# Kernel tuning notes

Hardware: AMD Instinct MI355X
Metric: run time of the kernel (lower is better)

## Reference

```python
import jax, jax.numpy as jnp
import numpy as np

B, S, H, NH = 2, 2048, 1024, 16
DH = H // NH  # 64

def setup_inputs() -> dict:
    key = jax.random.key(0)
    ks = jax.random.split(key, 6)
    return {
        "hidden_states": jax.random.normal(ks[0], (B, S, H), jnp.float32),
        "attention_mask": jnp.zeros((B, 1, 1, S), jnp.float32),  # additive mask (0 = attend)
        "local_attention_mask": jax.random.randint(ks[1], (B, 1, S, S), 0, 2).astype(jnp.int32),
        "gate_outputs": jax.random.uniform(ks[2], (B, NH, S, 1), jnp.float32),
        "Wq": jax.random.normal(ks[3], (H, H), jnp.float32) * 0.02,
        "bq": jnp.zeros((H,), jnp.float32),
        "Wk": jax.random.normal(ks[4], (H, H), jnp.float32) * 0.02,
        "bk": jnp.zeros((H,), jnp.float32),
        "Wv": jax.random.normal(ks[5], (H, H), jnp.float32) * 0.02,
        "bv": jnp.zeros((H,), jnp.float32),
    }

def _heads(x):
    # [B,S,H] -> [B,NH,S,DH]
    return x.reshape(B, S, NH, DH).transpose(0, 2, 1, 3)

def reference(hidden_states, attention_mask, local_attention_mask, gate_outputs, Wq, bq, Wk, bk, Wv, bv):
    q = _heads(hidden_states @ Wq.T + bq)
    k = _heads(hidden_states @ Wk.T + bk)
    v = _heads(hidden_states @ Wv.T + bv)
    scores = jnp.einsum("bhqd,bhkd->bhqk", q, k) / jnp.sqrt(jnp.float32(DH))
    # global branch (additive mask)
    probs_g = jax.nn.softmax(scores + attention_mask, axis=-1)
    ctx_g = jnp.einsum("bhqk,bhkd->bhqd", probs_g, v)
    # local branch: 0/1 mask -> additive -inf mask
    lmask = (1.0 - local_attention_mask.astype(jnp.float32)) * jnp.finfo(jnp.float32).min
    probs_l = jax.nn.softmax(scores + lmask, axis=-1)
    ctx_l = jnp.einsum("bhqk,bhkd->bhqd", probs_l, v)
    ctx = gate_outputs * ctx_l + (1.0 - gate_outputs) * ctx_g  # [B,NH,S,DH]
    return ctx.transpose(0, 2, 1, 3).reshape(B, S, H)
```

## Files before the change

### kernel.cpp

```cpp
#include <hip/hip_runtime.h>
#include <cstdint>
#include <cstddef>

typedef short short8 __attribute__((ext_vector_type(8)));
typedef float floatx4 __attribute__((ext_vector_type(4)));
typedef unsigned short ushort4v __attribute__((ext_vector_type(4)));
typedef unsigned int uintx4 __attribute__((ext_vector_type(4)));

constexpr int B_ = 2, S_ = 2048, H_ = 1024, NH_ = 16, DH_ = 64;
constexpr int K_ = H_;

__device__ __forceinline__ unsigned short f2bf(float f) {
  unsigned u = __float_as_uint(f);
  u += 0x7fffu + ((u >> 16) & 1u);
  return (unsigned short)(u >> 16);
}

__device__ __forceinline__ unsigned cvtpk(float a, float b) {
  unsigned r;
  asm("v_cvt_pk_bf16_f32 %0, %1, %2" : "=v"(r) : "v"(a), "v"(b));
  return r;
}

__global__ __launch_bounds__(256) void prep_kernel(
    const float* __restrict__ hs, unsigned short* __restrict__ hbf,
    const float* __restrict__ Wq, const float* __restrict__ Wk, const float* __restrict__ Wv,
    unsigned short* __restrict__ wqb, unsigned short* __restrict__ wkb,
    unsigned short* __restrict__ wvb,
    const int* __restrict__ lm, unsigned long long* __restrict__ bm,
    const float* __restrict__ am, float* __restrict__ ea) {
  const int bid = blockIdx.x, tid = threadIdx.x;
  if (bid < 1792) {
    const float* in;
    unsigned short* out;
    int off;
    if (bid < 1024) { in = hs; out = hbf; off = bid; }
    else {
      int wsel = (bid - 1024) >> 8;
      in = (wsel == 0) ? Wq : (wsel == 1) ? Wk : Wv;
      out = (wsel == 0) ? wqb : (wsel == 1) ? wkb : wvb;
      off = (bid - 1024) & 255;
    }
    const int base = off * 4096;
#pragma unroll
    for (int j = 0; j < 4; j++) {
      int i = base + j * 1024 + tid * 4;
      float4 v = *reinterpret_cast<const float4*>(in + i);
      ushort4v o;
      o.x = f2bf(v.x); o.y = f2bf(v.y); o.z = f2bf(v.z); o.w = f2bf(v.w);
      *reinterpret_cast<ushort4v*>(out + i) = o;
    }
  } else if (bid < 9984) {
    const int wbase = (bid - 1792) * 16 + (tid >> 6) * 4;
    const int lane = tid & 63;
#pragma unroll
    for (int j = 0; j < 4; j++) {
      unsigned long long bits = __ballot(lm[(size_t)(wbase + j) * 64 + lane] != 0);
      if (lane == 0) bm[wbase + j] = bits;
    }
  } else {
#pragma unroll
    for (int j = 0; j < 4; j++) {
      int i = j * 1024 + tid * 4;
      float4 v = *reinterpret_cast<const float4*>(am + i);
      float4 o;
      o.x = __expf(v.x); o.y = __expf(v.y); o.z = __expf(v.z); o.w = __expf(v.w);
      *reinterpret_cast<float4*>(ea + i) = o;
    }
  }
}

typedef __attribute__((address_space(1))) const void gvoid;
typedef __attribute__((address_space(3))) void lvoid;
__device__ __forceinline__ void async16(const unsigned short* gp, unsigned short* lp) {
  __builtin_amdgcn_global_load_lds((gvoid*)gp, (lvoid*)lp, 16, 0, 0);
}

__global__ __launch_bounds__(256) void gemm_qkv(
    const unsigned short* __restrict__ A,
    const unsigned short* __restrict__ Wq, const unsigned short* __restrict__ Wk,
    const unsigned short* __restrict__ Wv,
    const float* __restrict__ bq, const float* __restrict__ bk, const float* __restrict__ bv,
    unsigned short* __restrict__ qo, unsigned short* __restrict__ ko,
    unsigned short* __restrict__ vo) {
  __shared__ alignas(16) unsigned short As[128 * 32];
  __shared__ alignas(16) unsigned short Bs[128 * 32];
  const int z = blockIdx.z;
  const unsigned short* W = (z == 0) ? Wq : (z == 1) ? Wk : Wv;
  const float* bias = (z == 0) ? bq : (z == 1) ? bk : bv;

  const int m0 = blockIdx.x * 128, n0 = blockIdx.y * 128;
  const int tid = threadIdx.x, lane = tid & 63, wvi = tid >> 6;
  const int wr = wvi >> 1, wc = wvi & 1, quad = lane >> 4, l16 = lane & 15;

  floatx4 zf = {0.f, 0.f, 0.f, 0.f};
  floatx4 acc[4][4];
  for (int i = 0; i < 4; i++)
    for (int j = 0; j < 4; j++) acc[i][j] = zf;

  for (int kk = 0; kk < K_; kk += 32) {
#pragma unroll
    for (int i = 0; i < 2; i++) {
      int cb = wvi * 128 + i * 64;
      int c = cb + lane;
      int row = c >> 2, kc = c & 3;
      async16(A + (size_t)(m0 + row) * K_ + kk + kc * 8, As + cb * 8);
      async16(W + (size_t)(n0 + row) * K_ + kk + kc * 8, Bs + cb * 8);
    }
    __syncthreads();
    short8 af[4], bfr[4];
#pragma unroll
    for (int mf = 0; mf < 4; mf++)
      af[mf] = *reinterpret_cast<const short8*>(&As[(wr * 64 + mf * 16 + l16) * 32 + quad * 8]);
#pragma unroll
    for (int nf = 0; nf < 4; nf++)
      bfr[nf] = *reinterpret_cast<const short8*>(&Bs[(wc * 64 + nf * 16 + l16) * 32 + quad * 8]);
    if (z == 2) {
#pragma unroll
      for (int mf = 0; mf < 4; mf++)
#pragma unroll
        for (int nf = 0; nf < 4; nf++)
          acc[mf][nf] = __builtin_amdgcn_mfma_f32_16x16x32_bf16(af[mf], bfr[nf], acc[mf][nf], 0, 0, 0);
    } else {
#pragma unroll
      for (int mf = 0; mf < 4; mf++)
#pragma unroll
        for (int nf = 0; nf < 4; nf++)
          acc[mf][nf] = __builtin_amdgcn_mfma_f32_16x16x32_bf16(bfr[nf], af[mf], acc[mf][nf], 0, 0, 0);
    }
    __syncthreads();
  }

  if (z == 2) {
#pragma unroll
    for (int mf = 0; mf < 4; mf++) {
      int mbase = m0 + wr * 64 + mf * 16 + quad * 4;
      int b = mbase >> 11, s0 = mbase & 2047;
      int kl = s0 & 63;
#pragma unroll
      for (int nf = 0; nf < 4; nf++) {
        int n = n0 + wc * 64 + nf * 16 + l16;
        int h = n >> 6, d = n & 63;
        int bh = b * NH_ + h;
        float bvv = bias[n];
        floatx4 c = acc[mf][nf];
        size_t base = (size_t)bh * 131072 + (s0 >> 6) * 4096 + (d >> 4) * 1024 +
                      (kl >> 5) * 512 + ((kl >> 3) & 3) * 128 + (d & 15) * 8 + (kl & 7);
        ushort4v p;
        p.x = f2bf(c[0] + bvv); p.y = f2bf(c[1] + bvv);
        p.z = f2bf(c[2] + bvv); p.w = f2bf(c[3] + bvv);
        *reinterpret_cast<ushort4v*>(&vo[base]) = p;
      }
    }
  } else {
#pragma unroll
    for (int mf = 0; mf < 4; mf++) {
      int s = m0 + wr * 64 + mf * 16 + l16;
      int b = s >> 11;
      int sq = s & 2047;
#pragma unroll
      for (int nf = 0; nf < 4; nf++) {
        int nn = n0 + wc * 64 + nf * 16 + quad * 4;
        int h = nn >> 6, dh = nn & 63;
        int bh = b * NH_ + h;
        float4 b4 = *reinterpret_cast<const float4*>(bias + nn);
        floatx4 c = acc[mf][nf];
        if (z == 0) {
          ushort4v p;
          p.x = f2bf((c[0] + b4.x) * 0.18033688011112042f);
          p.y = f2bf((c[1] + b4.y) * 0.18033688011112042f);
          p.z = f2bf((c[2] + b4.z) * 0.18033688011112042f);
          p.w = f2bf((c[3] + b4.w) * 0.18033688011112042f);
          *reinterpret_cast<ushort4v*>(&qo[((size_t)bh * S_ + sq) * DH_ + dh]) = p;
        } else {
          int kl = sq & 63;
          int t = ((kl >> 4) & 2) | ((kl >> 2) & 1);
          int rr = ((kl >> 1) & 12) | (kl & 3);
          size_t base = (size_t)bh * 131072 + (sq >> 6) * 4096 + t * 1024 +
                        (dh >> 5) * 512 + ((dh >> 3) & 3) * 128 + rr * 8 + (dh & 7);
          ushort4v p;
          p.x = f2bf(c[0] + b4.x); p.y = f2bf(c[1] + b4.y);
          p.z = f2bf(c[2] + b4.z); p.w = f2bf(c[3] + b4.w);
          *reinterpret_cast<ushort4v*>(&ko[base]) = p;
        }
      }
    }
  }
}

__global__ __launch_bounds__(256, 4) void attn_kernel(
    const unsigned short* __restrict__ q,
    const unsigned short* __restrict__ kperm,
    const unsigned short* __restrict__ vperm,
    const float* __restrict__ eam,
    const unsigned long long* __restrict__ bm,
    const float* __restrict__ gate,
    float* __restrict__ out) {
  __shared__ alignas(16) unsigned short Ks[2][4096];
  __shared__ alignas(16) unsigned short Vs[2][4096];

  const int flat = blockIdx.x;
  const int h = (flat & 7) + 8 * ((flat >> 3) & 1);
  const int b = (flat >> 4) & 1;
  const int qt = flat >> 5;
  const int tid = threadIdx.x, lane = tid & 63, wvi = tid >> 6;
  const int quad = lane >> 4, l16 = lane & 15;
  const int bh = b * NH_ + h;
  const int q0 = qt * 64 + wvi * 16;
  const int quad8 = quad * 8;

  const unsigned short* qrow = q + ((size_t)bh * S_ + q0 + l16) * DH_;
  short8 qf0 = *reinterpret_cast<const short8*>(qrow + quad * 8);
  short8 qf1 = *reinterpret_cast<const short8*>(qrow + 32 + quad * 8);

  floatx4 zf = {0.f, 0.f, 0.f, 0.f};
  float psg = 0.f, psl = 0.f;
  floatx4 accg[4], accl[4];
#pragma unroll
  for (int i = 0; i < 4; i++) { accg[i] = zf; accl[i] = zf; }

  const unsigned short* kp = kperm + (size_t)bh * 131072;
  const unsigned short* vp = vperm + (size_t)bh * 131072;
  const float* eamb = eam + (size_t)b * S_;
  const unsigned long long* bmq = bm + ((size_t)b * S_ + q0 + l16) * (S_ / 64);

  const int soA = tid * 8, soB = 2048 + tid * 8;
  const unsigned short* kgA = kp + soA;
  const unsigned short* kgB = kp + soB;
  const unsigned short* vgA = vp + soA;
  const unsigned short* vgB = vp + soB;

  uint4 pk0 = *reinterpret_cast<const uint4*>(kgA);
  uint4 pk1 = *reinterpret_cast<const uint4*>(kgB);
  uint4 pv0 = *reinterpret_cast<const uint4*>(vgA);
  uint4 pv1 = *reinterpret_cast<const uint4*>(vgB);
  *reinterpret_cast<uint4*>(&Ks[0][soA]) = pk0;
  *reinterpret_cast<uint4*>(&Ks[0][soB]) = pk1;
  *reinterpret_cast<uint4*>(&Vs[0][soA]) = pv0;
  *reinterpret_cast<uint4*>(&Vs[0][soB]) = pv1;
  pk0 = *reinterpret_cast<const uint4*>(kgA + 4096);
  pk1 = *reinterpret_cast<const uint4*>(kgB + 4096);
  pv0 = *reinterpret_cast<const uint4*>(vgA + 4096);
  pv1 = *reinterpret_cast<const uint4*>(vgB + 4096);

  for (int kt = 0; kt < S_ / 64; kt++) {
    __syncthreads();
    {
      const int bn = (kt + 1) & 1;
      *reinterpret_cast<uint4*>(&Ks[bn][soA]) = pk0;
      *reinterpret_cast<uint4*>(&Ks[bn][soB]) = pk1;
      *reinterpret_cast<uint4*>(&Vs[bn][soA]) = pv0;
      *reinterpret_cast<uint4*>(&Vs[bn][soB]) = pv1;
    }
    {
      const int tb = ((kt + 2) & 31) * 4096;
      pk0 = *reinterpret_cast<const uint4*>(kgA + tb);
      pk1 = *reinterpret_cast<const uint4*>(kgB + tb);
      pv0 = *reinterpret_cast<const uint4*>(vgA + tb);
      pv1 = *reinterpret_cast<const uint4*>(vgB + tb);
    }
    const int k0 = kt * 64;
    uint2 wv = *reinterpret_cast<const uint2*>(&bmq[kt]);
    unsigned wq0 = wv.x >> quad8;
    unsigned wq1 = wv.y >> quad8;
    float4 ea0 = *reinterpret_cast<const float4*>(eamb + k0 + quad8);
    float4 ea1 = *reinterpret_cast<const float4*>(eamb + k0 + 4 + quad8);
    float4 ea2 = *reinterpret_cast<const float4*>(eamb + k0 + 32 + quad8);
    float4 ea3 = *reinterpret_cast<const float4*>(eamb + k0 + 36 + quad8);

    const unsigned short* Kc = Ks[kt & 1];
    const unsigned short* Vc = Vs[kt & 1];
    floatx4 scT[4];
#pragma unroll
    for (int t = 0; t < 4; t++) {
      const unsigned short* kr = Kc + t * 1024 + lane * 8;
      short8 kf0 = *reinterpret_cast<const short8*>(kr);
      short8 kf1 = *reinterpret_cast<const short8*>(kr + 512);
      scT[t] = __builtin_amdgcn_mfma_f32_16x16x32_bf16(kf0, qf0, zf, 0, 0, 0);
      scT[t] = __builtin_amdgcn_mfma_f32_16x16x32_bf16(kf1, qf1, scT[t], 0, 0, 0);
    }
    uintx4 fgv[2], flv[2];
#pragma unroll
    for (int t = 0; t < 4; t++) {
      const int T = t >> 1, tau = t & 1;
      floatx4 sc = scT[t];
      unsigned wq = T ? wq1 : wq0;
      float4 ea = (t == 0) ? ea0 : (t == 1) ? ea1 : (t == 2) ? ea2 : ea3;
      unsigned m4 = (wq >> (tau * 4)) & 0xFu;
      float e0 = __builtin_amdgcn_exp2f(sc[0]);
      float e1 = __builtin_amdgcn_exp2f(sc[1]);
      float e2 = __builtin_amdgcn_exp2f(sc[2]);
      float e3 = __builtin_amdgcn_exp2f(sc[3]);
      float g0 = e0 * ea.x, g1 = e1 * ea.y, g2 = e2 * ea.z, g3 = e3 * ea.w;
      psg += (g0 + g1) + (g2 + g3);
      float l0 = (m4 & 1u) ? e0 : 0.f;
      float l1 = (m4 & 2u) ? e1 : 0.f;
      float l2 = (m4 & 4u) ? e2 : 0.f;
      float l3 = (m4 & 8u) ? e3 : 0.f;
      psl += (l0 + l1) + (l2 + l3);
      fgv[T][tau * 2]     = cvtpk(g0, g1);
      fgv[T][tau * 2 + 1] = cvtpk(g2, g3);
      flv[T][tau * 2]     = cvtpk(l0, l1);
      flv[T][tau * 2 + 1] = cvtpk(l2, l3);
    }
    short8 FG0 = __builtin_bit_cast(short8, fgv[0]);
    short8 FG1 = __builtin_bit_cast(short8, fgv[1]);
    short8 FL0 = __builtin_bit_cast(short8, flv[0]);
    short8 FL1 = __builtin_bit_cast(short8, flv[1]);
#pragma unroll
    for (int d = 0; d < 4; d++) {
      const unsigned short* vb = Vc + d * 1024 + lane * 8;
      short8 v0 = *reinterpret_cast<const short8*>(vb);
      short8 v1 = *reinterpret_cast<const short8*>(vb + 512);
      accg[d] = __builtin_amdgcn_mfma_f32_16x16x32_bf16(v0, FG0, accg[d], 0, 0, 0);
      accl[d] = __builtin_amdgcn_mfma_f32_16x16x32_bf16(v0, FL0, accl[d], 0, 0, 0);
      accg[d] = __builtin_amdgcn_mfma_f32_16x16x32_bf16(v1, FG1, accg[d], 0, 0, 0);
      accl[d] = __builtin_amdgcn_mfma_f32_16x16x32_bf16(v1, FL1, accl[d], 0, 0, 0);
    }
  }

  float lgf = psg;
  lgf += __shfl_xor(lgf, 16, 64);
  lgf += __shfl_xor(lgf, 32, 64);
  float llf = psl;
  llf += __shfl_xor(llf, 16, 64);
  llf += __shfl_xor(llf, 32, 64);
  const int s = q0 + l16;
  const float g = gate[(size_t)bh * S_ + s];
  const float cg = (1.f - g) / lgf, cl = g / llf;
  float* orow = out + ((size_t)b * S_ + s) * H_ + h * DH_ + quad * 4;
#pragma unroll
  for (int d = 0; d < 4; d++) {
    float4 o;
    o.x = cl * accl[d][0] + cg * accg[d][0];
    o.y = cl * accl[d][1] + cg * accg[d][1];
    o.z = cl * accl[d][2] + cg * accg[d][2];
    o.w = cl * accl[d][3] + cg * accg[d][3];
    *reinterpret_cast<float4*>(orow + d * 16) = o;
  }
}

extern "C" void kernel_launch(void* const* d_in, const int* in_sizes, int n_in,
                              void* d_out, int out_size, void* d_ws, size_t ws_size,
                              hipStream_t stream) {
  (void)in_sizes; (void)n_in; (void)out_size; (void)ws_size;
  const float* hs = (const float*)d_in[0];
  const float* am = (const float*)d_in[1];
  const int* lm = (const int*)d_in[2];
  const float* gate = (const float*)d_in[3];
  const float* Wq = (const float*)d_in[4];
  const float* bq = (const float*)d_in[5];
  const float* Wk = (const float*)d_in[6];
  const float* bk = (const float*)d_in[7];
  const float* Wv = (const float*)d_in[8];
  const float* bv = (const float*)d_in[9];
  float* out = (float*)d_out;

  unsigned short* ws = (unsigned short*)d_ws;
  unsigned short* hbf = ws;
  unsigned short* wqb = hbf + 4194304;
  unsigned short* wkb = wqb + 1048576;
  unsigned short* wvb = wkb + 1048576;
  unsigned short* qb = wvb + 1048576;
  unsigned short* kb = qb + 4194304;
  unsigned short* vtb = kb + 4194304;
  unsigned long long* bmp = (unsigned long long*)(vtb + 4194304);
  float* eamp = (float*)(bmp + 131072);

  prep_kernel<<<9985, 256, 0, stream>>>(hs, hbf, Wq, Wk, Wv, wqb, wkb, wvb, lm, bmp, am, eamp);
  gemm_qkv<<<dim3(32, 8, 3), 256, 0, stream>>>(hbf, wqb, wkb, wvb, bq, bk, bv, qb, kb, vtb);
  attn_kernel<<<dim3(1024), 256, 0, stream>>>(qb, kb, vtb, eamp, bmp, gate, out);
}
```

Before: 229.5 us.

## Move mask preprocessing into GEMM launch and double K-step per sync

The local-mask bit-packing and attention-mask exponentiation blocks move out of the prep kernel and are appended as extra blocks of the QKV GEMM launch, so that memory-bound work can overlap with the GEMM tiles. The GEMM now loads 64 K-elements per iteration into two LDS halves, halving the number of barriers per tile. This doubles LDS use per block, which may lower occupancy. The 1D grid also reorders the GEMM tiles and puts the mask blocks after them, which could delay the GEMM's tail.

```diff
diff --git a/kernel.cpp b/kernel.cpp
--- a/kernel.cpp
+++ b/kernel.cpp
@@ -26,47 +26,26 @@
     const float* __restrict__ hs, unsigned short* __restrict__ hbf,
     const float* __restrict__ Wq, const float* __restrict__ Wk, const float* __restrict__ Wv,
     unsigned short* __restrict__ wqb, unsigned short* __restrict__ wkb,
-    unsigned short* __restrict__ wvb,
-    const int* __restrict__ lm, unsigned long long* __restrict__ bm,
-    const float* __restrict__ am, float* __restrict__ ea) {
+    unsigned short* __restrict__ wvb) {
   const int bid = blockIdx.x, tid = threadIdx.x;
-  if (bid < 1792) {
-    const float* in;
-    unsigned short* out;
-    int off;
-    if (bid < 1024) { in = hs; out = hbf; off = bid; }
-    else {
-      int wsel = (bid - 1024) >> 8;
-      in = (wsel == 0) ? Wq : (wsel == 1) ? Wk : Wv;
-      out = (wsel == 0) ? wqb : (wsel == 1) ? wkb : wvb;
-      off = (bid - 1024) & 255;
-    }
-    const int base = off * 4096;
-#pragma unroll
-    for (int j = 0; j < 4; j++) {
-      int i = base + j * 1024 + tid * 4;
-      float4 v = *reinterpret_cast<const float4*>(in + i);
-      ushort4v o;
-      o.x = f2bf(v.x); o.y = f2bf(v.y); o.z = f2bf(v.z); o.w = f2bf(v.w);
-      *reinterpret_cast<ushort4v*>(out + i) = o;
-    }
-  } else if (bid < 9984) {
-    const int wbase = (bid - 1792) * 16 + (tid >> 6) * 4;
-    const int lane = tid & 63;
-#pragma unroll
-    for (int j = 0; j < 4; j++) {
-      unsigned long long bits = __ballot(lm[(size_t)(wbase + j) * 64 + lane] != 0);
-      if (lane == 0) bm[wbase + j] = bits;
-    }
-  } else {
-#pragma unroll
-    for (int j = 0; j < 4; j++) {
-      int i = j * 1024 + tid * 4;
-      float4 v = *reinterpret_cast<const float4*>(am + i);
-      float4 o;
-      o.x = __expf(v.x); o.y = __expf(v.y); o.z = __expf(v.z); o.w = __expf(v.w);
-      *reinterpret_cast<float4*>(ea + i) = o;
-    }
+  const float* in;
+  unsigned short* out;
+  int off;
+  if (bid < 1024) { in = hs; out = hbf; off = bid; }
+  else {
+    int wsel = (bid - 1024) >> 8;
+    in = (wsel == 0) ? Wq : (wsel == 1) ? Wk : Wv;
+    out = (wsel == 0) ? wqb : (wsel == 1) ? wkb : wvb;
+    off = (bid - 1024) & 255;
+  }
+  const int base = off * 4096;
+#pragma unroll
+  for (int j = 0; j < 4; j++) {
+    int i = base + j * 1024 + tid * 4;
+    float4 v = *reinterpret_cast<const float4*>(in + i);
+    ushort4v o;
+    o.x = f2bf(v.x); o.y = f2bf(v.y); o.z = f2bf(v.z); o.w = f2bf(v.w);
+    *reinterpret_cast<ushort4v*>(out + i) = o;
   }
 }
 
@@ -82,15 +61,43 @@
     const unsigned short* __restrict__ Wv,
     const float* __restrict__ bq, const float* __restrict__ bk, const float* __restrict__ bv,
     unsigned short* __restrict__ qo, unsigned short* __restrict__ ko,
-    unsigned short* __restrict__ vo) {
-  __shared__ alignas(16) unsigned short As[128 * 32];
-  __shared__ alignas(16) unsigned short Bs[128 * 32];
-  const int z = blockIdx.z;
+    unsigned short* __restrict__ vo,
+    const int* __restrict__ lm, unsigned long long* __restrict__ bm,
+    const float* __restrict__ am, float* __restrict__ ea) {
+  __shared__ alignas(16) unsigned short As0[128 * 32];
+  __shared__ alignas(16) unsigned short As1[128 * 32];
+  __shared__ alignas(16) unsigned short Bs0[128 * 32];
+  __shared__ alignas(16) unsigned short Bs1[128 * 32];
+  const int bidf = blockIdx.x, tid = threadIdx.x;
+
+  if (bidf >= 768) {
+    if (bidf < 8960) {
+      const int wbase = (bidf - 768) * 16 + (tid >> 6) * 4;
+      const int lane = tid & 63;
+#pragma unroll
+      for (int j = 0; j < 4; j++) {
+        unsigned long long bits = __ballot(lm[(size_t)(wbase + j) * 64 + lane] != 0);
+        if (lane == 0) bm[wbase + j] = bits;
+      }
+    } else {
+#pragma unroll
+      for (int j = 0; j < 4; j++) {
+        int i = j * 1024 + tid * 4;
+        float4 v = *reinterpret_cast<const float4*>(am + i);
+        float4 o;
+        o.x = __expf(v.x); o.y = __expf(v.y); o.z = __expf(v.z); o.w = __expf(v.w);
+        *reinterpret_cast<float4*>(ea + i) = o;
+      }
+    }
+    return;
+  }
+
+  const int z = bidf >> 8;
   const unsigned short* W = (z == 0) ? Wq : (z == 1) ? Wk : Wv;
   const float* bias = (z == 0) ? bq : (z == 1) ? bk : bv;
 
-  const int m0 = blockIdx.x * 128, n0 = blockIdx.y * 128;
-  const int tid = threadIdx.x, lane = tid & 63, wvi = tid >> 6;
+  const int m0 = (bidf & 31) * 128, n0 = ((bidf >> 5) & 7) * 128;
+  const int lane = tid & 63, wvi = tid >> 6;
   const int wr = wvi >> 1, wc = wvi & 1, quad = lane >> 4, l16 = lane & 15;
 
   floatx4 zf = {0.f, 0.f, 0.f, 0.f};
@@ -98,35 +105,44 @@
   for (int i = 0; i < 4; i++)
     for (int j = 0; j < 4; j++) acc[i][j] = zf;
 
-  for (int kk = 0; kk < K_; kk += 32) {
+  for (int kk = 0; kk < K_; kk += 64) {
 #pragma unroll
     for (int i = 0; i < 2; i++) {
       int cb = wvi * 128 + i * 64;
       int c = cb + lane;
       int row = c >> 2, kc = c & 3;
-      async16(A + (size_t)(m0 + row) * K_ + kk + kc * 8, As + cb * 8);
-      async16(W + (size_t)(n0 + row) * K_ + kk + kc * 8, Bs + cb * 8);
+      const unsigned short* Ar = A + (size_t)(m0 + row) * K_ + kk + kc * 8;
+      const unsigned short* Wr = W + (size_t)(n0 + row) * K_ + kk + kc * 8;
+      async16(Ar, As0 + cb * 8);
+      async16(Wr, Bs0 + cb * 8);
+      async16(Ar + 32, As1 + cb * 8);
+      async16(Wr + 32, Bs1 + cb * 8);
     }
     __syncthreads();
-    short8 af[4], bfr[4];
-#pragma unroll
-    for (int mf = 0; mf < 4; mf++)
-      af[mf] = *reinterpret_cast<const short8*>(&As[(wr * 64 + mf * 16 + l16) * 32 + quad * 8]);
-#pragma unroll
-    for (int nf = 0; nf < 4; nf++)
-      bfr[nf] = *reinterpret_cast<const short8*>(&Bs[(wc * 64 + nf * 16 + l16) * 32 + quad * 8]);
-    if (z == 2) {
+#pragma unroll
+    for (int ks = 0; ks < 2; ks++) {
+      const unsigned short* Ah = ks ? As1 : As0;
+      const unsigned short* Bh = ks ? Bs1 : Bs0;
+      short8 af[4], bfr[4];
 #pragma unroll
       for (int mf = 0; mf < 4; mf++)
-#pragma unroll
-        for (int nf = 0; nf < 4; nf++)
-          acc[mf][nf] = __builtin_amdgcn_mfma_f32_16x16x32_bf16(af[mf], bfr[nf], acc[mf][nf], 0, 0, 0);
-    } else {
-#pragma unroll
-      for (int mf = 0; mf < 4; mf++)
-#pragma unroll
-        for (int nf = 0; nf < 4; nf++)
-          acc[mf][nf] = __builtin_amdgcn_mfma_f32_16x16x32_bf16(bfr[nf], af[mf], acc[mf][nf], 0, 0, 0);
+        af[mf] = *reinterpret_cast<const short8*>(&Ah[(wr * 64 + mf * 16 + l16) * 32 + quad * 8]);
+#pragma unroll
+      for (int nf = 0; nf < 4; nf++)
+        bfr[nf] = *reinterpret_cast<const short8*>(&Bh[(wc * 64 + nf * 16 + l16) * 32 + quad * 8]);
+      if (z == 2) {
+#pragma unroll
+        for (int mf = 0; mf < 4; mf++)
+#pragma unroll
+          for (int nf = 0; nf < 4; nf++)
+            acc[mf][nf] = __builtin_amdgcn_mfma_f32_16x16x32_bf16(af[mf], bfr[nf], acc[mf][nf], 0, 0, 0);
+      } else {
+#pragma unroll
+        for (int mf = 0; mf < 4; mf++)
+#pragma unroll
+          for (int nf = 0; nf < 4; nf++)
+            acc[mf][nf] = __builtin_amdgcn_mfma_f32_16x16x32_bf16(bfr[nf], af[mf], acc[mf][nf], 0, 0, 0);
+      }
     }
     __syncthreads();
   }
@@ -367,7 +383,8 @@
   unsigned long long* bmp = (unsigned long long*)(vtb + 4194304);
   float* eamp = (float*)(bmp + 131072);
 
-  prep_kernel<<<9985, 256, 0, stream>>>(hs, hbf, Wq, Wk, Wv, wqb, wkb, wvb, lm, bmp, am, eamp);
-  gemm_qkv<<<dim3(32, 8, 3), 256, 0, stream>>>(hbf, wqb, wkb, wvb, bq, bk, bv, qb, kb, vtb);
+  prep_kernel<<<1792, 256, 0, stream>>>(hs, hbf, Wq, Wk, Wv, wqb, wkb, wvb);
+  gemm_qkv<<<8961, 256, 0, stream>>>(hbf, wqb, wkb, wvb, bq, bk, bv, qb, kb, vtb,
+                                     lm, bmp, am, eamp);
   attn_kernel<<<dim3(1024), 256, 0, stream>>>(qb, kb, vtb, eamp, bmp, gate, out);
 }
```

Result: slower. 234.3 us (+2.1%).

## Double-buffer QKV GEMM with narrower N tile and prioritize attention MFMA

Applied to the files above, without the earlier changes.

The QKV projection GEMM gets two LDS buffers, so the next K-slice loads asynchronously while the current one is multiplied. Each iteration now needs one barrier instead of two. The N tile shrinks from 128 to 64, which doubles the grid to 1536 blocks and lets launch bounds request higher occupancy. The cost is less operand reuse per block. Separately, the attention kernel raises wave priority around its MFMA sections to improve interleaving between waves.

```diff
diff --git a/kernel.cpp b/kernel.cpp
--- a/kernel.cpp
+++ b/kernel.cpp
@@ -76,56 +76,67 @@
   __builtin_amdgcn_global_load_lds((gvoid*)gp, (lvoid*)lp, 16, 0, 0);
 }
 
-__global__ __launch_bounds__(256) void gemm_qkv(
+__global__ __launch_bounds__(256, 6) void gemm_qkv(
     const unsigned short* __restrict__ A,
     const unsigned short* __restrict__ Wq, const unsigned short* __restrict__ Wk,
     const unsigned short* __restrict__ Wv,
     const float* __restrict__ bq, const float* __restrict__ bk, const float* __restrict__ bv,
     unsigned short* __restrict__ qo, unsigned short* __restrict__ ko,
     unsigned short* __restrict__ vo) {
-  __shared__ alignas(16) unsigned short As[128 * 32];
-  __shared__ alignas(16) unsigned short Bs[128 * 32];
+  __shared__ alignas(16) unsigned short As[2][128 * 32];
+  __shared__ alignas(16) unsigned short Bs[2][64 * 32];
   const int z = blockIdx.z;
   const unsigned short* W = (z == 0) ? Wq : (z == 1) ? Wk : Wv;
   const float* bias = (z == 0) ? bq : (z == 1) ? bk : bv;
 
-  const int m0 = blockIdx.x * 128, n0 = blockIdx.y * 128;
+  const int m0 = blockIdx.x * 128, n0 = blockIdx.y * 64;
   const int tid = threadIdx.x, lane = tid & 63, wvi = tid >> 6;
   const int wr = wvi >> 1, wc = wvi & 1, quad = lane >> 4, l16 = lane & 15;
 
   floatx4 zf = {0.f, 0.f, 0.f, 0.f};
-  floatx4 acc[4][4];
+  floatx4 acc[4][2];
   for (int i = 0; i < 4; i++)
-    for (int j = 0; j < 4; j++) acc[i][j] = zf;
-
-  for (int kk = 0; kk < K_; kk += 32) {
-#pragma unroll
-    for (int i = 0; i < 2; i++) {
-      int cb = wvi * 128 + i * 64;
-      int c = cb + lane;
-      int row = c >> 2, kc = c & 3;
-      async16(A + (size_t)(m0 + row) * K_ + kk + kc * 8, As + cb * 8);
-      async16(W + (size_t)(n0 + row) * K_ + kk + kc * 8, Bs + cb * 8);
-    }
-    __syncthreads();
-    short8 af[4], bfr[4];
+    for (int j = 0; j < 2; j++) acc[i][j] = zf;
+
+  const int cbA0 = wvi * 128, cbA1 = wvi * 128 + 64, cbB = wvi * 64;
+  const int cA0 = cbA0 + lane, cA1 = cbA1 + lane, cB = cbB + lane;
+  const unsigned short* Ag0 = A + (size_t)(m0 + (cA0 >> 2)) * K_ + (cA0 & 3) * 8;
+  const unsigned short* Ag1 = A + (size_t)(m0 + (cA1 >> 2)) * K_ + (cA1 & 3) * 8;
+  const unsigned short* Wg  = W + (size_t)(n0 + (cB >> 2)) * K_ + (cB & 3) * 8;
+
+  auto STAGE = [&](int t) {
+    const int bn = t & 1;
+    const int kk = t * 32;
+    async16(Ag0 + kk, &As[bn][cbA0 * 8]);
+    async16(Ag1 + kk, &As[bn][cbA1 * 8]);
+    async16(Wg + kk, &Bs[bn][cbB * 8]);
+  };
+
+  STAGE(0);
+  __syncthreads();
+
+  for (int kt = 0; kt < 32; kt++) {
+    if (kt != 31) STAGE(kt + 1);
+    const unsigned short* Ah = As[kt & 1];
+    const unsigned short* Bh = Bs[kt & 1];
+    short8 af[4], bfr[2];
 #pragma unroll
     for (int mf = 0; mf < 4; mf++)
-      af[mf] = *reinterpret_cast<const short8*>(&As[(wr * 64 + mf * 16 + l16) * 32 + quad * 8]);
-#pragma unroll
-    for (int nf = 0; nf < 4; nf++)
-      bfr[nf] = *reinterpret_cast<const short8*>(&Bs[(wc * 64 + nf * 16 + l16) * 32 + quad * 8]);
+      af[mf] = *reinterpret_cast<const short8*>(&Ah[(wr * 64 + mf * 16 + l16) * 32 + quad * 8]);
+#pragma unroll
+    for (int nf = 0; nf < 2; nf++)
+      bfr[nf] = *reinterpret_cast<const short8*>(&Bh[(wc * 32 + nf * 16 + l16) * 32 + quad * 8]);
     if (z == 2) {
 #pragma unroll
       for (int mf = 0; mf < 4; mf++)
 #pragma unroll
-        for (int nf = 0; nf < 4; nf++)
+        for (int nf = 0; nf < 2; nf++)
           acc[mf][nf] = __builtin_amdgcn_mfma_f32_16x16x32_bf16(af[mf], bfr[nf], acc[mf][nf], 0, 0, 0);
     } else {
 #pragma unroll
       for (int mf = 0; mf < 4; mf++)
 #pragma unroll
-        for (int nf = 0; nf < 4; nf++)
+        for (int nf = 0; nf < 2; nf++)
           acc[mf][nf] = __builtin_amdgcn_mfma_f32_16x16x32_bf16(bfr[nf], af[mf], acc[mf][nf], 0, 0, 0);
     }
     __syncthreads();
@@ -138,8 +149,8 @@
       int b = mbase >> 11, s0 = mbase & 2047;
       int kl = s0 & 63;
 #pragma unroll
-      for (int nf = 0; nf < 4; nf++) {
-        int n = n0 + wc * 64 + nf * 16 + l16;
+      for (int nf = 0; nf < 2; nf++) {
+        int n = n0 + wc * 32 + nf * 16 + l16;
         int h = n >> 6, d = n & 63;
         int bh = b * NH_ + h;
         float bvv = bias[n];
@@ -159,8 +170,8 @@
       int b = s >> 11;
       int sq = s & 2047;
 #pragma unroll
-      for (int nf = 0; nf < 4; nf++) {
-        int nn = n0 + wc * 64 + nf * 16 + quad * 4;
+      for (int nf = 0; nf < 2; nf++) {
+        int nn = n0 + wc * 32 + nf * 16 + quad * 4;
         int h = nn >> 6, dh = nn & 63;
         int bh = b * NH_ + h;
         float4 b4 = *reinterpret_cast<const float4*>(bias + nn);
@@ -271,6 +282,7 @@
     const unsigned short* Kc = Ks[kt & 1];
     const unsigned short* Vc = Vs[kt & 1];
     floatx4 scT[4];
+    __builtin_amdgcn_s_setprio(1);
 #pragma unroll
     for (int t = 0; t < 4; t++) {
       const unsigned short* kr = Kc + t * 1024 + lane * 8;
@@ -279,6 +291,7 @@
       scT[t] = __builtin_amdgcn_mfma_f32_16x16x32_bf16(kf0, qf0, zf, 0, 0, 0);
       scT[t] = __builtin_amdgcn_mfma_f32_16x16x32_bf16(kf1, qf1, scT[t], 0, 0, 0);
     }
+    __builtin_amdgcn_s_setprio(0);
     uintx4 fgv[2], flv[2];
 #pragma unroll
     for (int t = 0; t < 4; t++) {
@@ -307,6 +320,7 @@
     short8 FG1 = __builtin_bit_cast(short8, fgv[1]);
     short8 FL0 = __builtin_bit_cast(short8, flv[0]);
     short8 FL1 = __builtin_bit_cast(short8, flv[1]);
+    __builtin_amdgcn_s_setprio(1);
 #pragma unroll
     for (int d = 0; d < 4; d++) {
       const unsigned short* vb = Vc + d * 1024 + lane * 8;
@@ -317,6 +331,7 @@
       accg[d] = __builtin_amdgcn_mfma_f32_16x16x32_bf16(v1, FG1, accg[d], 0, 0, 0);
       accl[d] = __builtin_amdgcn_mfma_f32_16x16x32_bf16(v1, FL1, accl[d], 0, 0, 0);
     }
+    __builtin_amdgcn_s_setprio(0);
   }
 
   float lgf = psg;
@@ -368,6 +383,6 @@
   float* eamp = (float*)(bmp + 131072);
 
   prep_kernel<<<9985, 256, 0, stream>>>(hs, hbf, Wq, Wk, Wv, wqb, wkb, wvb, lm, bmp, am, eamp);
-  gemm_qkv<<<dim3(32, 8, 3), 256, 0, stream>>>(hbf, wqb, wkb, wvb, bq, bk, bv, qb, kb, vtb);
+  gemm_qkv<<<dim3(32, 16, 3), 256, 0, stream>>>(hbf, wqb, wkb, wvb, bq, bk, bv, qb, kb, vtb);
   attn_kernel<<<dim3(1024), 256, 0, stream>>>(qb, kb, vtb, eamp, bmp, gate, out);
 }
```

Measured after the change: 345.4 us. 1.5x slower.
